# Kernel tuning notes

Hardware: AMD Instinct MI355X
Metric: run time of the kernel (lower is better)

The kernel has to match this reference:

```python
import jax, jax.numpy as jnp
import numpy as np

N = 50000      # nodes
E = 800000     # edges
IN = 64        # in_channels
HID = 256      # hidden_dim
LAT = 64       # latent_dim
KS = 2         # kernel_size per dim
DIM = 3        # pseudo-coordinate dim
K = KS ** DIM  # 8 spline weight matrices


def spline_basis_coeffs(pseudo, ks, dim, dtype):
    """Degree-1 open B-spline basis: returns per-edge coefficients c [E, ks**dim]."""
    e = pseudo.shape[0]
    v = pseudo * (ks - 1)                                   # [E, dim]
    bot = jnp.clip(jnp.floor(v), 0, ks - 1).astype(jnp.int32)
    frac = v - bot
    c = jnp.zeros((e, ks ** dim), dtype)
    rows = jnp.arange(e)
    for s in range(2 ** dim):  # 8 knot combinations (fixed small loop)
        w = jnp.ones(e, dtype)
        idx = jnp.zeros(e, jnp.int32)
        for d in range(dim):
            bit = (s >> d) & 1
            w = w * (frac[:, d] if bit else 1.0 - frac[:, d])
            idx = idx + jnp.clip(bot[:, d] + bit, 0, ks - 1) * (ks ** d)
        c = c.at[rows, idx].add(w)
    return c


def spline_conv(x, edge_index, pseudo, W, Wroot, b):
    """SplineConv with aggr='mean', root weight and bias (degree-1 open splines)."""
    src, dst = edge_index[0], edge_index[1]
    n = x.shape[0]
    e = pseudo.shape[0]
    c = spline_basis_coeffs(pseudo, KS, DIM, x.dtype)        # [E, K]
    x_src = x[src]                                           # [E, in] gather
    deg = jax.ops.segment_sum(jnp.ones(e, x.dtype), dst, num_segments=n)
    inv_deg = (1.0 / jnp.maximum(deg, 1.0))[:, None]         # [N, 1] mean aggr
    out = jnp.zeros((n, W.shape[2]), x.dtype)
    for k in range(W.shape[0]):  # K=8 fixed loop; scatter-add then dense matmul
        agg = jax.ops.segment_sum(c[:, k:k + 1] * x_src, dst, num_segments=n)
        out = out + (agg * inv_deg) @ W[k]
    return out + x @ Wroot + b


def setup_inputs() -> dict:
    key = jax.random.key(0)
    ks = jax.random.split(key, 12)
    x = jax.random.normal(ks[0], (N, IN), jnp.float32)
    edge_index = jax.random.randint(ks[1], (2, E), 0, N, jnp.int32)
    s = 0.05
    return {
        "x": x,
        "edge_index": edge_index,
        "conv1_W": jax.random.normal(ks[2], (K, IN, HID), jnp.float32) * s,
        "conv1_root": jax.random.normal(ks[3], (IN, HID), jnp.float32) * s,
        "conv1_b": jnp.zeros((HID,), jnp.float32),
        "conv2_W": jax.random.normal(ks[4], (K, HID, LAT), jnp.float32) * s,
        "conv2_root": jax.random.normal(ks[5], (HID, LAT), jnp.float32) * s,
        "conv2_b": jnp.zeros((LAT,), jnp.float32),
        "dec_w1": jax.random.normal(ks[6], (LAT, HID), jnp.float32) * s,
        "dec_b1": jnp.zeros((HID,), jnp.float32),
        "dec_w2": jax.random.normal(ks[7], (HID, IN), jnp.float32) * s,
        "dec_b2": jnp.zeros((IN,), jnp.float32),
    }


def reference(x, edge_index, conv1_W, conv1_root, conv1_b,
              conv2_W, conv2_root, conv2_b,
              dec_w1, dec_b1, dec_w2, dec_b2):
    pseudo = jnp.zeros((edge_index.shape[1], DIM), x.dtype)  # forward builds zeros
    h = jax.nn.relu(spline_conv(x, edge_index, pseudo, conv1_W, conv1_root, conv1_b))
    z = spline_conv(h, edge_index, pseudo, conv2_W, conv2_root, conv2_b)
    h2 = jax.nn.relu(z @ dec_w1 + dec_b1)
    return h2 @ dec_w2 + dec_b2
```

## Files before the change

kernel.cpp:

```cpp
#include <hip/hip_runtime.h>
#include <hip/hip_bf16.h>


#define THREADS 256

typedef __attribute__((ext_vector_type(8))) short bf16x8;
typedef __attribute__((ext_vector_type(4))) float f32x4;

__device__ __forceinline__ float bf2f(unsigned short u) {
    unsigned v = ((unsigned)u) << 16;
    return __builtin_bit_cast(float, v);
}
__device__ __forceinline__ unsigned short f2bf(float f) {
    __hip_bfloat16 h = __float2bfloat16(f);
    return __builtin_bit_cast(unsigned short, h);
}
__device__ __forceinline__ void acc8(float* f, uint4 v) {
    f[0] += bf2f((unsigned short)v.x); f[1] += bf2f((unsigned short)(v.x >> 16));
    f[2] += bf2f((unsigned short)v.y); f[3] += bf2f((unsigned short)(v.y >> 16));
    f[4] += bf2f((unsigned short)v.z); f[5] += bf2f((unsigned short)(v.z >> 16));
    f[6] += bf2f((unsigned short)v.w); f[7] += bf2f((unsigned short)(v.w >> 16));
}

__device__ __forceinline__ void pack_one(unsigned short* dst,
                                         const float* W0, const float* W1,
                                         int NB, int ksplit, int colsplit,
                                         int ld0, int ld1, int t) {
    int i = t & 7, lane = (t >> 3) & 63, rest = t >> 9;
    int j = rest % NB, s = rest / NB;
    int k = s * 32 + ((lane >> 4) << 3) + i;
    int c = (j << 4) + (lane & 15);
    float v;
    if (c >= colsplit)    v = W1[(size_t)k * ld1 + (c - colsplit)];
    else if (k >= ksplit) v = W1[(size_t)(k - ksplit) * ld1 + c];
    else                  v = W0[(size_t)k * ld0 + c];
    dst[t] = f2bf(v);
}

#define BIG (1 << 30)

__global__ void prep_kernel(const float* __restrict__ W1g, const float* __restrict__ root1,
                            const float* __restrict__ W2g, const float* __restrict__ root2,
                            const float* __restrict__ dw1, const float* __restrict__ dw2,
                            const float* __restrict__ x, const int* __restrict__ dstv,
                            int* __restrict__ bcnt,
                            unsigned short* __restrict__ Pb1,
                            unsigned short* __restrict__ Pb2,
                            unsigned short* __restrict__ Pd1,
                            unsigned short* __restrict__ Pd2,
                            unsigned short* __restrict__ ab1,
                            unsigned short* __restrict__ xh,
                            int n, int np, int E, int pb_pack) {
    if ((int)blockIdx.x >= pb_pack) {
        __shared__ int hist[256];
        int t = threadIdx.x;
        hist[t] = 0;
        __syncthreads();
        int e0 = ((int)blockIdx.x - pb_pack) * 4096;
#pragma unroll
        for (int i = 0; i < 16; ++i) {
            int e = e0 + t + i * 256;
            if (e < E) atomicAdd(&hist[dstv[e] >> 8], 1);
        }
        __syncthreads();
        int h = hist[t];
        if (h) atomicAdd(&bcnt[t], h);
        return;
    }
    int t = blockIdx.x * blockDim.x + threadIdx.x;
    if (t < 32768) {
        pack_one(Pb1, W1g, root1, 16, 64, BIG, 256, 256, t);
    } else if (t < 65536) {
        pack_one(Pb2, W2g, root2, 8, BIG, 64, 64, 64, t - 32768);
    } else if (t < 81920) {
        pack_one(Pd1, dw1, dw1, 16, BIG, BIG, 256, 256, t - 65536);
    } else if (t < 98304) {
        pack_one(Pd2, dw2, dw2, 4, BIG, BIG, 64, 64, t - 81920);
    } else if (t < 98304 + n * 16) {
        int u = t - 98304;
        int row = u >> 4, c4 = (u & 15) * 4;
        float4 v = *(const float4*)(x + (size_t)row * 64 + c4);
        unsigned lo = (unsigned)f2bf(v.x) | ((unsigned)f2bf(v.y) << 16);
        unsigned hi = (unsigned)f2bf(v.z) | ((unsigned)f2bf(v.w) << 16);
        uint2 o; o.x = lo; o.y = hi;
        *(uint2*)(ab1 + (size_t)row * 128 + 64 + c4) = o;
        int hh = c4 >> 5, off = c4 & 31;
        *(uint2*)(xh + (size_t)hh * np * 32 + (size_t)row * 32 + off) = o;
    }
}

__global__ __launch_bounds__(512) void partition_edges(
    const int* __restrict__ src, const int* __restrict__ dst,
    const int* __restrict__ bcnt, int* __restrict__ bcur,
    int* __restrict__ epack, int E) {
    __shared__ int hist[256];
    __shared__ int base[256];
    __shared__ int lcur[256];
    __shared__ int bb[256];
    int t = threadIdx.x;
    if (t < 256) { hist[t] = 0; lcur[t] = 0; }
    __syncthreads();
    int e0 = blockIdx.x * 2048;
    int myd[4], mys[4];
#pragma unroll
    for (int i = 0; i < 4; ++i) {
        int e = e0 + t + i * 512;
        int d = (e < E) ? dst[e] : -1;
        mys[i] = (e < E) ? src[e] : 0;
        myd[i] = d;
        if (d >= 0) atomicAdd(&hist[d >> 8], 1);
    }
    int cb = 0;
    if (t < 256) { cb = bcnt[t]; bb[t] = cb; }
    __syncthreads();
    for (int off = 1; off < 256; off <<= 1) {
        int xv = (t >= off && t < 256) ? bb[t - off] : 0;
        __syncthreads();
        if (t < 256) bb[t] += xv;
        __syncthreads();
    }
    if (t < 256) {
        int h = hist[t];
        if (h > 0) base[t] = (bb[t] - cb) + atomicAdd(&bcur[t], h);
    }
    __syncthreads();
#pragma unroll
    for (int i = 0; i < 4; ++i) {
        int d = myd[i];
        if (d >= 0) {
            int b = d >> 8;
            int p = atomicAdd(&lcur[b], 1);
            epack[base[b] + p] = ((d & 255) << 20) | mys[i];
        }
    }
}

__global__ __launch_bounds__(1024) void bucket_fill2(
    const int* __restrict__ epack, const int* __restrict__ bcnt,
    int* __restrict__ offs, float* __restrict__ invd,
    int* __restrict__ esrc, int N) {
    __shared__ int sb_[256];
    __shared__ int nh[256];
    __shared__ int loff[256];
    __shared__ int ncur[256];
    __shared__ int stage[8192];
    int b = blockIdx.x, t = threadIdx.x;
    int n0 = b << 8;
    int cb = 0;
    if (t < 256) { cb = bcnt[t]; sb_[t] = cb; }
    __syncthreads();
    for (int off = 1; off < 256; off <<= 1) {
        int xv = (t >= off && t < 256) ? sb_[t - off] : 0;
        __syncthreads();
        if (t < 256) sb_[t] += xv;
        __syncthreads();
    }
    int ebase = b ? sb_[b - 1] : 0;
    int ecount = sb_[b] - ebase;
    if (b == 0 && t == 0) offs[N] = sb_[255];
    if (t < 256) nh[t] = 0;
    __syncthreads();
    for (int i = t; i < ecount; i += 1024)
        atomicAdd(&nh[epack[ebase + i] >> 20], 1);
    __syncthreads();
    int v = 0;
    if (t < 256) { v = nh[t]; loff[t] = v; }
    __syncthreads();
    for (int off = 1; off < 256; off <<= 1) {
        int xv = (t >= off && t < 256) ? loff[t - off] : 0;
        __syncthreads();
        if (t < 256) loff[t] += xv;
        __syncthreads();
    }
    if (t < 256) {
        int ex = loff[t] - v;
        loff[t] = ex;
        int node = n0 + t;
        if (node < N) {
            offs[node] = ebase + ex;
            invd[node] = 1.0f / (float)max(v, 1);
        }
        ncur[t] = 0;
    }
    __syncthreads();
    bool useLds = (ecount <= 8192);
    for (int i = t; i < ecount; i += 1024) {
        int p = epack[ebase + i];
        int dl = p >> 20;
        int pos = atomicAdd(&ncur[dl], 1);
        int g = loff[dl] + pos;
        int sv = p & 0xFFFFF;
        if (useLds) stage[g] = sv;
        else        esrc[ebase + g] = sv;
    }
    __syncthreads();
    if (useLds)
        for (int i = t; i < ecount; i += 1024) esrc[ebase + i] = stage[i];
}

template <int MODE>
__global__ __launch_bounds__(256) void agg_half(
    const unsigned short* __restrict__ tbl,
    const int* __restrict__ esrc, const int* __restrict__ offs,
    const float* __restrict__ invd,
    const unsigned short* __restrict__ hrootb,
    const float* __restrict__ b2,
    unsigned short* __restrict__ outb, int n, int np) {
    const int h = blockIdx.x & 1;
    const int node = (blockIdx.x >> 1) * 4 + (threadIdx.x >> 6);
    if (node >= n) return;
    const int l = threadIdx.x & 63;
    const int slot = l >> 2, c = l & 3;
    const unsigned short* tb = tbl + (size_t)h * np * 32 + c * 8;
    int s0 = offs[node], e0 = offs[node + 1];
    float a[8] = {};
    for (int j = s0 + slot; __any(j < e0); j += 16) {
        if (j < e0) {
            int src = esrc[j];
            uint4 v = *(const uint4*)(tb + (size_t)src * 32);
            acc8(a, v);
        }
    }
#pragma unroll
    for (int k = 0; k < 8; ++k) {
        a[k] += __shfl_xor(a[k], 4);
        a[k] += __shfl_xor(a[k], 8);
        a[k] += __shfl_xor(a[k], 16);
        a[k] += __shfl_xor(a[k], 32);
    }
    if (slot == 0) {
        float iv = invd[node];
        float v[8];
#pragma unroll
        for (int k = 0; k < 8; ++k) v[k] = a[k] * iv;
        int fo = h * 32 + c * 8;
        if (MODE == 1) {
            uint4 hr = *(const uint4*)(hrootb + (size_t)node * 64 + fo);
            float4 bA = *(const float4*)(b2 + fo);
            float4 bB = *(const float4*)(b2 + fo + 4);
            v[0] += bf2f((unsigned short)hr.x)         + bA.x;
            v[1] += bf2f((unsigned short)(hr.x >> 16)) + bA.y;
            v[2] += bf2f((unsigned short)hr.y)         + bA.z;
            v[3] += bf2f((unsigned short)(hr.y >> 16)) + bA.w;
            v[4] += bf2f((unsigned short)hr.z)         + bB.x;
            v[5] += bf2f((unsigned short)(hr.z >> 16)) + bB.y;
            v[6] += bf2f((unsigned short)hr.w)         + bB.z;
            v[7] += bf2f((unsigned short)(hr.w >> 16)) + bB.w;
        }
        unsigned p0 = (unsigned)f2bf(v[0]) | ((unsigned)f2bf(v[1]) << 16);
        unsigned p1 = (unsigned)f2bf(v[2]) | ((unsigned)f2bf(v[3]) << 16);
        unsigned p2 = (unsigned)f2bf(v[4]) | ((unsigned)f2bf(v[5]) << 16);
        unsigned p3 = (unsigned)f2bf(v[6]) | ((unsigned)f2bf(v[7]) << 16);
        uint4 o; o.x = p0; o.y = p1; o.z = p2; o.w = p3;
        const int OS = (MODE == 0) ? 128 : 64;
        *(uint4*)(outb + (size_t)node * OS + fo) = o;
    }
}

template <int K1, int NBW2, int OUTM>
__global__ __launch_bounds__(256) void gemm_fused(
    const unsigned short* __restrict__ A,
    const unsigned short* __restrict__ Bp1, const float* __restrict__ bias1,
    const unsigned short* __restrict__ Bp2, const float* __restrict__ bias2,
    void* __restrict__ Cv, unsigned short* __restrict__ Cv2, int n, int np)
{
    constexpr int KS1 = K1 / 32;
    constexpr int NB2 = NBW2 * 4;
    __shared__ unsigned short ht[64][264];

    const int m0 = blockIdx.x * 64;
    const int lane = threadIdx.x & 63;
    const int w = threadIdx.x >> 6;
    const int quad = lane >> 4;
    const int l16 = lane & 15;

    {
        f32x4 acc[4][4] = {};
        const unsigned short* Arow = A + (size_t)(m0 + l16) * K1 + quad * 8;
        for (int s = 0; s < KS1; ++s) {
            bf16x8 a[4];
#pragma unroll
            for (int mb = 0; mb < 4; ++mb)
                a[mb] = *(const bf16x8*)(Arow + (size_t)mb * 16 * K1 + s * 32);
#pragma unroll
            for (int jn = 0; jn < 4; ++jn) {
                int j = w * 4 + jn;
                bf16x8 b = *(const bf16x8*)(Bp1 + ((size_t)(s * 16 + j) * 64 + lane) * 8);
#pragma unroll
                for (int mb = 0; mb < 4; ++mb)
                    acc[mb][jn] = __builtin_amdgcn_mfma_f32_16x16x32_bf16(a[mb], b, acc[mb][jn], 0, 0, 0);
            }
        }
#pragma unroll
        for (int jn = 0; jn < 4; ++jn) {
            int col = (w * 4 + jn) * 16 + l16;
            float bv = bias1[col];
#pragma unroll
            for (int mb = 0; mb < 4; ++mb)
#pragma unroll
                for (int r = 0; r < 4; ++r) {
                    int row = mb * 16 + quad * 4 + r;
                    ht[row][col] = f2bf(fmaxf(acc[mb][jn][r] + bv, 0.f));
                }
        }
    }
    __syncthreads();

    {
        f32x4 acc[4][NBW2] = {};
        for (int s = 0; s < 8; ++s) {
            bf16x8 a[4];
#pragma unroll
            for (int mb = 0; mb < 4; ++mb)
                a[mb] = *(const bf16x8*)&ht[mb * 16 + l16][s * 32 + quad * 8];
#pragma unroll
            for (int jn = 0; jn < NBW2; ++jn) {
                int j = w * NBW2 + jn;
                bf16x8 b = *(const bf16x8*)(Bp2 + ((size_t)(s * NB2 + j) * 64 + lane) * 8);
#pragma unroll
                for (int mb = 0; mb < 4; ++mb)
                    acc[mb][jn] = __builtin_amdgcn_mfma_f32_16x16x32_bf16(a[mb], b, acc[mb][jn], 0, 0, 0);
            }
        }
#pragma unroll
        for (int jn = 0; jn < NBW2; ++jn) {
            int col = (w * NBW2 + jn) * 16 + l16;
            float bv = bias2 ? bias2[col] : 0.f;
#pragma unroll
            for (int mb = 0; mb < 4; ++mb)
#pragma unroll
                for (int r = 0; r < 4; ++r) {
                    int row = m0 + mb * 16 + quad * 4 + r;
                    if (row < n) {
                        float vv = acc[mb][jn][r] + bv;
                        if (OUTM == 1) {
                            unsigned short val = f2bf(vv);
                            if (col < 64)
                                ((unsigned short*)Cv)[(size_t)(col >> 5) * np * 32 +
                                                      (size_t)row * 32 + (col & 31)] = val;
                            else
                                Cv2[(size_t)row * 64 + (col - 64)] = val;
                        } else {
                            ((float*)Cv)[(size_t)row * 64 + col] = vv;
                        }
                    }
                }
        }
    }
}

extern "C" void kernel_launch(void* const* d_in, const int* in_sizes, int n_in,
                              void* d_out, int out_size, void* d_ws, size_t ws_size,
                              hipStream_t stream) {
    const float* x      = (const float*)d_in[0];
    const int*   ei     = (const int*)d_in[1];
    const float* W1g    = (const float*)d_in[2];
    const float* root1  = (const float*)d_in[3];
    const float* b1     = (const float*)d_in[4];
    const float* W2g    = (const float*)d_in[5];
    const float* root2  = (const float*)d_in[6];
    const float* b2     = (const float*)d_in[7];
    const float* dw1    = (const float*)d_in[8];
    const float* db1    = (const float*)d_in[9];
    const float* dw2    = (const float*)d_in[10];
    const float* db2    = (const float*)d_in[11];
    float* out = (float*)d_out;

    const int N = in_sizes[0] / 64;
    const int E = in_sizes[1] / 2;
    const int Npad = N + 64;
    const int* srcv = ei;
    const int* dstv = ei + E;

    char* ws = (char*)d_ws;
    auto alloc = [&](size_t bytes) -> void* {
        void* p = (void*)ws;
        ws += (bytes + 255) & ~(size_t)255;
        return p;
    };
    int*   bcnt   = (int*)alloc(1024);
    int*   bcur   = (int*)alloc(1024);
    int*   offs   = (int*)alloc((size_t)(N + 1) * 4);
    float* invd   = (float*)alloc((size_t)N * 4);
    int*   esrc   = (int*)alloc((size_t)E * 4);
    int*   epack  = (int*)alloc((size_t)E * 4);
    unsigned short* Pb1 = (unsigned short*)alloc(32768 * 2);
    unsigned short* Pb2 = (unsigned short*)alloc(32768 * 2);
    unsigned short* Pd1 = (unsigned short*)alloc(16384 * 2);
    unsigned short* Pd2 = (unsigned short*)alloc(16384 * 2);
    unsigned short* ab1    = (unsigned short*)alloc((size_t)Npad * 128 * 2);
    unsigned short* xh     = (unsigned short*)alloc((size_t)2 * Npad * 32 * 2);
    unsigned short* hwh    = (unsigned short*)alloc((size_t)2 * Npad * 32 * 2);
    unsigned short* hrootb = (unsigned short*)alloc((size_t)Npad * 64 * 2);
    unsigned short* z      = (unsigned short*)alloc((size_t)Npad * 64 * 2);

    hipMemsetAsync(bcnt, 0, 2048, stream);

    int gb = (N + 63) / 64;
    int nbkt = (N + 255) / 256;
    int pa = (E + 4095) / 4096;
    int pa2 = (E + 2047) / 2048;
    int pb_pack = (98304 + N * 16 + THREADS - 1) / THREADS;
    int nb2 = ((N + 3) / 4) * 2;

    prep_kernel<<<pb_pack + pa, THREADS, 0, stream>>>(
        W1g, root1, W2g, root2, dw1, dw2, x, dstv, bcnt,
        Pb1, Pb2, Pd1, Pd2, ab1, xh, N, Npad, E, pb_pack);
    partition_edges<<<pa2, 512, 0, stream>>>(srcv, dstv, bcnt, bcur, epack, E);
    bucket_fill2<<<nbkt, 1024, 0, stream>>>(epack, bcnt, offs, invd, esrc, N);

    agg_half<0><<<nb2, THREADS, 0, stream>>>(xh, esrc, offs, invd,
                                             nullptr, nullptr, ab1, N, Npad);
    gemm_fused<128, 2, 1><<<gb, 256, 0, stream>>>(ab1, Pb1, b1, Pb2, nullptr,
                                                  hwh, hrootb, N, Npad);
    agg_half<1><<<nb2, THREADS, 0, stream>>>(hwh, esrc, offs, invd,
                                             hrootb, b2, z, N, Npad);
    gemm_fused<64, 1, 0><<<gb, 256, 0, stream>>>(z, Pd1, db1, Pd2, db2,
                                                 out, nullptr, N, Npad);
}
```

Measured before the change: 241.6 us.

## Pin aggregation feature halves to XCC parity via atomic work queues

The aggregation kernel now reads the hardware XCC id. It picks the feature half from the XCC parity and takes node groups from a per-half atomic counter, instead of deriving both from blockIdx. Each XCC's L2 then only ever gathers rows from one half of the bf16 feature table, shrinking the per-XCC working set so it can stay cache-resident. Edge indices, offsets, root terms and outputs also switch to nontemporal loads and stores to avoid polluting cache. The risk is that correctness relies on blocks splitting evenly between even and odd XCCs. The extra atomic and syncthreads per block add a little overhead.

```diff
diff --git a/kernel.cpp b/kernel.cpp
--- a/kernel.cpp
+++ b/kernel.cpp
@@ -6,6 +6,7 @@
 
 typedef __attribute__((ext_vector_type(8))) short bf16x8;
 typedef __attribute__((ext_vector_type(4))) float f32x4;
+typedef __attribute__((ext_vector_type(4))) unsigned int u32x4;
 
 __device__ __forceinline__ float bf2f(unsigned short u) {
     unsigned v = ((unsigned)u) << 16;
@@ -20,6 +21,17 @@
     f[2] += bf2f((unsigned short)v.y); f[3] += bf2f((unsigned short)(v.y >> 16));
     f[4] += bf2f((unsigned short)v.z); f[5] += bf2f((unsigned short)(v.z >> 16));
     f[6] += bf2f((unsigned short)v.w); f[7] += bf2f((unsigned short)(v.w >> 16));
+}
+__device__ __forceinline__ void acc8v(float* f, u32x4 v) {
+    f[0] += bf2f((unsigned short)v.x); f[1] += bf2f((unsigned short)(v.x >> 16));
+    f[2] += bf2f((unsigned short)v.y); f[3] += bf2f((unsigned short)(v.y >> 16));
+    f[4] += bf2f((unsigned short)v.z); f[5] += bf2f((unsigned short)(v.z >> 16));
+    f[6] += bf2f((unsigned short)v.w); f[7] += bf2f((unsigned short)(v.w >> 16));
+}
+__device__ __forceinline__ int get_xcc() {
+    int v;
+    asm volatile("s_getreg_b32 %0, hwreg(HW_REG_XCC_ID)" : "=s"(v));
+    return v;
 }
 
 __device__ __forceinline__ void pack_one(unsigned short* dst,
@@ -199,24 +211,34 @@
 }
 
 template <int MODE>
-__global__ __launch_bounds__(256) void agg_half(
+__global__ __launch_bounds__(256) void agg_q(
     const unsigned short* __restrict__ tbl,
     const int* __restrict__ esrc, const int* __restrict__ offs,
     const float* __restrict__ invd,
     const unsigned short* __restrict__ hrootb,
     const float* __restrict__ b2,
-    unsigned short* __restrict__ outb, int n, int np) {
-    const int h = blockIdx.x & 1;
-    const int node = (blockIdx.x >> 1) * 4 + (threadIdx.x >> 6);
+    unsigned short* __restrict__ outb, int* __restrict__ qctr,
+    int n, int np, int ngroups) {
+    __shared__ int sh[2];
+    if (threadIdx.x == 0) {
+        int half = get_xcc() & 1;
+        sh[0] = half;
+        sh[1] = atomicAdd(&qctr[half], 1);
+    }
+    __syncthreads();
+    const int h = sh[0], g = sh[1];
+    if (g >= ngroups) return;
+    const int node = g * 4 + (threadIdx.x >> 6);
     if (node >= n) return;
     const int l = threadIdx.x & 63;
     const int slot = l >> 2, c = l & 3;
     const unsigned short* tb = tbl + (size_t)h * np * 32 + c * 8;
-    int s0 = offs[node], e0 = offs[node + 1];
+    int s0 = __builtin_nontemporal_load(offs + node);
+    int e0 = __builtin_nontemporal_load(offs + node + 1);
     float a[8] = {};
     for (int j = s0 + slot; __any(j < e0); j += 16) {
         if (j < e0) {
-            int src = esrc[j];
+            int src = __builtin_nontemporal_load(esrc + j);
             uint4 v = *(const uint4*)(tb + (size_t)src * 32);
             acc8(a, v);
         }
@@ -235,7 +257,8 @@
         for (int k = 0; k < 8; ++k) v[k] = a[k] * iv;
         int fo = h * 32 + c * 8;
         if (MODE == 1) {
-            uint4 hr = *(const uint4*)(hrootb + (size_t)node * 64 + fo);
+            u32x4 hr = __builtin_nontemporal_load(
+                (const u32x4*)(hrootb + (size_t)node * 64 + fo));
             float4 bA = *(const float4*)(b2 + fo);
             float4 bB = *(const float4*)(b2 + fo + 4);
             v[0] += bf2f((unsigned short)hr.x)         + bA.x;
@@ -247,13 +270,13 @@
             v[6] += bf2f((unsigned short)hr.w)         + bB.z;
             v[7] += bf2f((unsigned short)(hr.w >> 16)) + bB.w;
         }
-        unsigned p0 = (unsigned)f2bf(v[0]) | ((unsigned)f2bf(v[1]) << 16);
-        unsigned p1 = (unsigned)f2bf(v[2]) | ((unsigned)f2bf(v[3]) << 16);
-        unsigned p2 = (unsigned)f2bf(v[4]) | ((unsigned)f2bf(v[5]) << 16);
-        unsigned p3 = (unsigned)f2bf(v[6]) | ((unsigned)f2bf(v[7]) << 16);
-        uint4 o; o.x = p0; o.y = p1; o.z = p2; o.w = p3;
+        u32x4 o;
+        o.x = (unsigned)f2bf(v[0]) | ((unsigned)f2bf(v[1]) << 16);
+        o.y = (unsigned)f2bf(v[2]) | ((unsigned)f2bf(v[3]) << 16);
+        o.z = (unsigned)f2bf(v[4]) | ((unsigned)f2bf(v[5]) << 16);
+        o.w = (unsigned)f2bf(v[6]) | ((unsigned)f2bf(v[7]) << 16);
         const int OS = (MODE == 0) ? 128 : 64;
-        *(uint4*)(outb + (size_t)node * OS + fo) = o;
+        __builtin_nontemporal_store(o, (u32x4*)(outb + (size_t)node * OS + fo));
     }
 }
 
@@ -380,6 +403,7 @@
     };
     int*   bcnt   = (int*)alloc(1024);
     int*   bcur   = (int*)alloc(1024);
+    int*   qctr   = (int*)alloc(256);
     int*   offs   = (int*)alloc((size_t)(N + 1) * 4);
     float* invd   = (float*)alloc((size_t)N * 4);
     int*   esrc   = (int*)alloc((size_t)E * 4);
@@ -394,14 +418,14 @@
     unsigned short* hrootb = (unsigned short*)alloc((size_t)Npad * 64 * 2);
     unsigned short* z      = (unsigned short*)alloc((size_t)Npad * 64 * 2);
 
-    hipMemsetAsync(bcnt, 0, 2048, stream);
+    hipMemsetAsync(bcnt, 0, 2304, stream);
 
     int gb = (N + 63) / 64;
     int nbkt = (N + 255) / 256;
     int pa = (E + 4095) / 4096;
     int pa2 = (E + 2047) / 2048;
     int pb_pack = (98304 + N * 16 + THREADS - 1) / THREADS;
-    int nb2 = ((N + 3) / 4) * 2;
+    int ngrp = (N + 3) / 4;
 
     prep_kernel<<<pb_pack + pa, THREADS, 0, stream>>>(
         W1g, root1, W2g, root2, dw1, dw2, x, dstv, bcnt,
@@ -409,12 +433,14 @@
     partition_edges<<<pa2, 512, 0, stream>>>(srcv, dstv, bcnt, bcur, epack, E);
     bucket_fill2<<<nbkt, 1024, 0, stream>>>(epack, bcnt, offs, invd, esrc, N);
 
-    agg_half<0><<<nb2, THREADS, 0, stream>>>(xh, esrc, offs, invd,
-                                             nullptr, nullptr, ab1, N, Npad);
+    agg_q<0><<<ngrp * 2, THREADS, 0, stream>>>(xh, esrc, offs, invd,
+                                               nullptr, nullptr, ab1,
+                                               qctr, N, Npad, ngrp);
     gemm_fused<128, 2, 1><<<gb, 256, 0, stream>>>(ab1, Pb1, b1, Pb2, nullptr,
                                                   hwh, hrootb, N, Npad);
-    agg_half<1><<<nb2, THREADS, 0, stream>>>(hwh, esrc, offs, invd,
-                                             hrootb, b2, z, N, Npad);
+    agg_q<1><<<ngrp * 2, THREADS, 0, stream>>>(hwh, esrc, offs, invd,
+                                               hrootb, b2, z,
+                                               qctr + 2, N, Npad, ngrp);
     gemm_fused<64, 1, 0><<<gb, 256, 0, stream>>>(z, Pd1, db1, Pd2, db2,
                                                  out, nullptr, N, Npad);
 }
```

Result: slower. 744.4 us (+208.1%).
